# Kernel tuning notes

Hardware: AMD Instinct MI355X
Metric: run time of the kernel (lower is better)

The kernel has to match this reference:

```python
import jax, jax.numpy as jnp
import numpy as np

H = W = 28
NUM_COUNTS = 10  # iteration counts 0..9, one per logit of determine_n


def conv2d(x, w, b=None, pad=2):
    # x: [B,C,H,W], w: [O,I,5,5]
    y = jax.lax.conv_general_dilated(
        x, w, window_strides=(1, 1), padding=[(pad, pad), (pad, pad)],
        dimension_numbers=("NCHW", "OIHW", "NCHW"))
    if b is not None:
        y = y + b[None, :, None, None]
    return y


def maxpool3(x):
    # kernel 3, stride 3, valid: 28 -> 9
    return jax.lax.reduce_window(
        x, -jnp.inf, jax.lax.max,
        window_dimensions=(1, 1, 3, 3), window_strides=(1, 1, 3, 3),
        padding="VALID")


def setup_inputs() -> dict:
    key = jax.random.key(0)
    ks = jax.random.split(key, 8)
    B = 4096
    s = 0.1
    return {
        "x": jax.random.normal(ks[0], (B, H * W), dtype=jnp.float32),
        "w1": jax.random.normal(ks[1], (8, 1, 5, 5), dtype=jnp.float32) * s,
        "b1": jax.random.normal(ks[2], (8,), dtype=jnp.float32) * s,
        "w2": jax.random.normal(ks[3], (16, 8, 5, 5), dtype=jnp.float32) * s,
        "b2": jax.random.normal(ks[4], (16,), dtype=jnp.float32) * s,
        "fcw": jax.random.normal(ks[5], (10, 16 * 9 * 9), dtype=jnp.float32) * s,
        "fcb": jax.random.normal(ks[6], (10,), dtype=jnp.float32) * s,
        "iterw": jax.random.normal(ks[7], (1, 1, 5, 5), dtype=jnp.float32) * s,
    }


def reference(x, w1, b1, w2, b2, fcw, fcb, iterw):
    B = x.shape[0]
    xi = x.reshape(B, 1, H, W)
    # determine_n: CNN router producing 10 logits over iteration counts
    h = jax.nn.relu(conv2d(xi, w1, b1))
    h = jax.nn.relu(conv2d(h, w2, b2))
    h = maxpool3(h).reshape(B, -1)                      # [B, 1296]
    logits = h @ fcw.T + fcb                            # [B, 10]
    probs = jax.nn.softmax(logits, axis=-1)             # [B, 10]
    # smooth TmIter: expected value over f^n(base), n = 0..9
    def step(y, _):
        return conv2d(y, iterw, None), y
    _, ys = jax.lax.scan(step, xi, None, length=NUM_COUNTS)  # [10,B,1,28,28]
    out = jnp.einsum("bn,nbchw->bchw", probs, ys)
    return out.reshape(B, H, W)
```

## Files before the change

kernel.cpp:

```cpp
#include <hip/hip_runtime.h>
#include <hip/hip_bf16.h>
#include <math.h>
#include <float.h>

typedef __fp16 f16x8  __attribute__((ext_vector_type(8)));
typedef __fp16 f16x2  __attribute__((ext_vector_type(2)));
typedef float  f32x16 __attribute__((ext_vector_type(16)));
typedef float  f32x4  __attribute__((ext_vector_type(4)));
typedef unsigned int u32x4 __attribute__((ext_vector_type(4)));
typedef unsigned int u32x2 __attribute__((ext_vector_type(2)));

__device__ inline f16x2 as_h2(unsigned u) { union { unsigned x; f16x2 h; } c; c.x = u; return c.h; }
__device__ inline unsigned pack2(float lo, float hi) {
    union { f16x2 h; unsigned x; } c; c.h[0] = (__fp16)lo; c.h[1] = (__fp16)hi; return c.x;
}
__device__ inline float dot2f(unsigned a, unsigned b, float acc) {
#if __has_builtin(__builtin_amdgcn_fdot2)
    return __builtin_amdgcn_fdot2(as_h2(a), as_h2(b), acc, false);
#else
    f16x2 ah = as_h2(a), bh = as_h2(b);
    return fmaf((float)ah[1], (float)bh[1], fmaf((float)ah[0], (float)bh[0], acc));
#endif
}
#define ALIGN16(hi, lo) __builtin_amdgcn_alignbit((hi), (lo), 16)

#define DY_TAB 0xA524A509A502A540ULL
#define DX_TAB 0x446A444A44924924ULL

__global__ __launch_bounds__(256, 4) void k1_router(
    const float* __restrict__ xg,
    const float* __restrict__ w1g,
    const float* __restrict__ b1g,
    const float* __restrict__ w2g,
    const float* __restrict__ b2g,
    const float* __restrict__ fcwg,
    const float* __restrict__ fcbg,
    float* __restrict__ wsp)
{
    __shared__ __align__(16) char lds[27120];
    char*   spadh  = lds;
    char*   wpk    = lds + 2560;
    __fp16* sh1T   = (__fp16*)(lds + 3200);
    __fp16* sw2t   = (__fp16*)(lds + 20560);
    float*  pooled = (float*)(lds + 20560);
    float*  swred  = (float*)(lds + 26960);

    const int tid  = threadIdx.x;
    const int b    = blockIdx.x;
    const int lane = tid & 63;
    const int wid  = tid >> 6;

    f32x4 z4 = {0.f, 0.f, 0.f, 0.f};
    for (int i = tid; i < 160; i += 256)  ((f32x4*)spadh)[i] = z4;
    for (int i = tid; i < 1085; i += 256) ((f32x4*)sh1T)[i] = z4;
    for (int i = tid; i < 400; i += 256) {
        const int tap = i >> 4, ch = i & 15;
        f16x8 v;
        #pragma unroll
        for (int j = 0; j < 8; ++j) v[j] = (__fp16)w2g[ch * 200 + j * 25 + tap];
        *((f16x8*)(sw2t + i * 8)) = v;
    }
    if (tid < 40) {
        const int r = tid >> 3, c = tid & 7;
        const float* w = w1g + c * 25 + r * 5;
        u32x4 W;
        W.x = pack2(w[0], w[1]); W.y = pack2(w[2], w[3]); W.z = pack2(w[4], 0.f); W.w = 0u;
        *((u32x4*)(wpk + tid * 16)) = W;
    }
    const int yy = tid / 7, q = tid - yy * 7;
    if (tid < 196) {
        f32x4 v = *((const f32x4*)(xg + (size_t)b * 784 + yy * 28 + q * 4));
        unsigned* dst = (unsigned*)(spadh + (yy + 2) * 80 + q * 8 + 4);
        dst[0] = pack2(v[0], v[1]); dst[1] = pack2(v[2], v[3]);
    }
    __syncthreads();

    if (tid < 196) {
        float o[8][4];
        #pragma unroll
        for (int c = 0; c < 8; ++c) {
            const float bv = b1g[c];
            #pragma unroll
            for (int px = 0; px < 4; ++px) o[c][px] = bv;
        }
        #pragma unroll
        for (int r = 0; r < 5; ++r) {
            const char* rowb = spadh + (yy + r) * 80 + q * 8;
            u32x2 A = *((const u32x2*)rowb);
            u32x2 B = *((const u32x2*)(rowb + 8));
            unsigned C0 = *((const unsigned*)(rowb + 16));
            unsigned P[8] = { A.x, ALIGN16(A.y, A.x), A.y, ALIGN16(B.x, A.y),
                              B.x, ALIGN16(B.y, B.x), B.y, ALIGN16(C0,  B.y) };
            #pragma unroll
            for (int c = 0; c < 8; ++c) {
                const u32x4 W = *((const u32x4*)(wpk + (r * 8 + c) * 16));
                #pragma unroll
                for (int px = 0; px < 4; ++px) {
                    float t = o[c][px];
                    t = dot2f(P[px],     W.x, t);
                    t = dot2f(P[px + 2], W.y, t);
                    t = dot2f(P[px + 4], W.z, t);
                    o[c][px] = t;
                }
            }
        }
        #pragma unroll
        for (int px = 0; px < 4; ++px) {
            f16x8 hv;
            #pragma unroll
            for (int c = 0; c < 8; ++c) hv[c] = (__fp16)fmaxf(o[c][px], 0.f);
            *((f16x8*)(sh1T + ((yy + 2) * 35 + (q * 4 + px + 2)) * 8)) = hv;
        }
    }
    const int lr = lane & 31;
    const int g2 = lane >> 5;
    int band = (lr * 57) >> 9; band = band > 2 ? 2 : band;
    const int dy = (int)((DY_TAB >> (2 * lr)) & 3ull);
    const int dx = (int)((DX_TAB >> (2 * lr)) & 3ull);
    const float biasv = (lr < 16) ? b2g[lr] : 0.f;

    f16x8 bfrag[13];
    int   toffB[13];
    #pragma unroll
    for (int s = 0; s < 13; ++s) {
        const int tap = 2 * s + g2;
        const int tapc = tap > 24 ? 24 : tap;
        f16x8 v = *((const f16x8*)(sw2t + (tapc * 16 + (lr & 15)) * 8));
        if (tap > 24 || lr >= 16) {
            #pragma unroll
            for (int j = 0; j < 8; ++j) v[j] = (__fp16)0.f;
        }
        bfrag[s] = v;
        const int ky = (tapc * 13) >> 6;
        const int kx = tapc - 5 * ky;
        toffB[s] = (ky * 35 + kx) * 16;
    }
    __syncthreads();

    auto tileBase = [&](int tile) -> const char* {
        const int cell = tile * 3 + band;
        const int cy = (cell * 57) >> 9, cx = cell - 9 * cy;
        return (const char*)sh1T + ((3 * cy + dy) * 35 + (3 * cx + dx)) * 16;
    };
    auto epi = [&](const f32x16& acc, int tile) {
        float mA, mB, mC;
        if (g2 == 0) {
            mA = fmaxf(fmaxf(fmaxf(acc[0],acc[1]),fmaxf(acc[2],acc[3])), acc[4]);
            mB = fmaxf(fmaxf(fmaxf(acc[5],acc[6]),acc[7]), fmaxf(acc[8],acc[9]));
            mC = fmaxf(fmaxf(fmaxf(acc[10],acc[11]),acc[12]), fmaxf(acc[13],acc[14]));
        } else {
            mA = fmaxf(fmaxf(acc[0],acc[1]),fmaxf(acc[2],acc[3]));
            mB = fmaxf(fmaxf(acc[4],acc[5]),fmaxf(acc[6],acc[7]));
            mC = fmaxf(fmaxf(acc[8],acc[9]),fmaxf(acc[10],acc[11]));
        }
        mA = fmaxf(mA, 0.f); mB = fmaxf(mB, 0.f); mC = fmaxf(mC, 0.f);
        mA = fmaxf(mA, __shfl_xor(mA, 32, 64));
        mB = fmaxf(mB, __shfl_xor(mB, 32, 64));
        mC = fmaxf(mC, __shfl_xor(mC, 32, 64));
        if (g2 == 0 && lr < 16) {
            pooled[lr * 81 + tile * 3 + 0] = mA;
            pooled[lr * 81 + tile * 3 + 1] = mB;
            pooled[lr * 81 + tile * 3 + 2] = mC;
        }
    };
    #pragma unroll 1
    for (int base = wid; base + 4 < 27; base += 8) {
        const char* a0 = tileBase(base);
        const char* a1 = tileBase(base + 4);
        f32x16 acc0, acc1;
        #pragma unroll
        for (int r = 0; r < 16; ++r) { acc0[r] = biasv; acc1[r] = biasv; }
        #pragma unroll
        for (int s = 0; s < 13; ++s) {
            f16x8 af0 = *((const f16x8*)(a0 + toffB[s]));
            f16x8 af1 = *((const f16x8*)(a1 + toffB[s]));
            acc0 = __builtin_amdgcn_mfma_f32_32x32x16_f16(af0, bfrag[s], acc0, 0, 0, 0);
            acc1 = __builtin_amdgcn_mfma_f32_32x32x16_f16(af1, bfrag[s], acc1, 0, 0, 0);
        }
        epi(acc0, base);
        epi(acc1, base + 4);
    }
    if (wid < 3) {
        const int tile = wid + 24;
        const char* a0 = tileBase(tile);
        f32x16 acc;
        #pragma unroll
        for (int r = 0; r < 16; ++r) acc[r] = biasv;
        #pragma unroll
        for (int s = 0; s < 13; ++s) {
            f16x8 af = *((const f16x8*)(a0 + toffB[s]));
            acc = __builtin_amdgcn_mfma_f32_32x32x16_f16(af, bfrag[s], acc, 0, 0, 0);
        }
        epi(acc, tile);
    }
    __syncthreads();

    {
        float part[10];
        #pragma unroll
        for (int j = 0; j < 10; ++j) part[j] = 0.f;
        for (int i4 = tid; i4 < 324; i4 += 256) {
            const f32x4 pv = ((const f32x4*)pooled)[i4];
            #pragma unroll
            for (int j = 0; j < 10; ++j) {
                const f32x4 fw = *((const f32x4*)(fcwg + j * 1296 + i4 * 4));
                part[j] = fmaf(pv[0], fw[0], part[j]);
                part[j] = fmaf(pv[1], fw[1], part[j]);
                part[j] = fmaf(pv[2], fw[2], part[j]);
                part[j] = fmaf(pv[3], fw[3], part[j]);
            }
        }
        #pragma unroll
        for (int j = 0; j < 10; ++j) {
            float v = part[j];
            #pragma unroll
            for (int off = 32; off > 0; off >>= 1) v += __shfl_down(v, off, 64);
            if (lane == 0) swred[wid * 10 + j] = v;
        }
    }
    __syncthreads();

    if (tid == 0) {
        float lg[10]; float mx = -FLT_MAX;
        #pragma unroll
        for (int j = 0; j < 10; ++j) {
            lg[j] = swred[j] + swred[10 + j] + swred[20 + j] + swred[30 + j] + fcbg[j];
            mx = fmaxf(mx, lg[j]);
        }
        float sum = 0.f; float e[10];
        #pragma unroll
        for (int j = 0; j < 10; ++j) { e[j] = expf(lg[j] - mx); sum += e[j]; }
        const float inv = 1.f / sum;
        #pragma unroll
        for (int j = 0; j < 10; ++j) wsp[(size_t)b * 16 + j] = e[j] * inv;
    }
}

__global__ __launch_bounds__(64, 4) void k2_scan(
    const float* __restrict__ xg,
    const float* __restrict__ iwg,
    const float* __restrict__ wsp,
    float* __restrict__ outg)
{
    __shared__ __align__(16) char arena[5120];
    char* bufA = arena;
    char* bufB = arena + 2560;

    const int tid = threadIdx.x;
    const int b   = blockIdx.x;

    f32x4 z4 = {0.f, 0.f, 0.f, 0.f};
    for (int i = tid; i < 320; i += 64) ((f32x4*)arena)[i] = z4;
    __syncthreads();

    for (int i = tid; i < 196; i += 64) {
        const int yy = i / 7, q = i - yy * 7;
        f32x4 v = *((const f32x4*)(xg + (size_t)b * 784 + yy * 28 + q * 4));
        unsigned* dst = (unsigned*)(bufA + (yy + 2) * 80 + q * 8 + 4);
        dst[0] = pack2(v[0], v[1]); dst[1] = pack2(v[2], v[3]);
    }
    __syncthreads();

    unsigned wp[5][3];
    #pragma unroll
    for (int r = 0; r < 5; ++r) {
        wp[r][0] = pack2(iwg[r * 5 + 0], iwg[r * 5 + 1]);
        wp[r][1] = pack2(iwg[r * 5 + 2], iwg[r * 5 + 3]);
        wp[r][2] = pack2(iwg[r * 5 + 4], 0.f);
    }

    const int rq = tid / 7, qq = tid - rq * 7;
    const float p0 = wsp[(size_t)b * 16];
    float accv[16];
    #pragma unroll
    for (int i = 0; i < 16; ++i) accv[i] = 0.f;

    const char* cur = bufA;
    char* nxt = bufB;
    #pragma unroll 1
    for (int n = 1; n <= 9; ++n) {
        const float pn = wsp[(size_t)b * 16 + n];
        if (tid < 49) {
            float v[4][4];
            #pragma unroll
            for (int rr = 0; rr < 4; ++rr)
                #pragma unroll
                for (int px = 0; px < 4; ++px) v[rr][px] = 0.f;
            #pragma unroll
            for (int r = 0; r < 8; ++r) {
                const char* rowb = cur + (4 * rq + r) * 80 + qq * 8;
                u32x2 A = *((const u32x2*)rowb);
                u32x2 B = *((const u32x2*)(rowb + 8));
                unsigned C0 = *((const unsigned*)(rowb + 16));
                unsigned P[8] = { A.x, ALIGN16(A.y, A.x), A.y, ALIGN16(B.x, A.y),
                                  B.x, ALIGN16(B.y, B.x), B.y, ALIGN16(C0,  B.y) };
                if (n == 1 && r >= 2 && r <= 5) {
                    f16x2 t1 = as_h2(A.y), t2 = as_h2(B.x);
                    accv[(r - 2) * 4 + 0] = p0 * (float)t1[0];
                    accv[(r - 2) * 4 + 1] = p0 * (float)t1[1];
                    accv[(r - 2) * 4 + 2] = p0 * (float)t2[0];
                    accv[(r - 2) * 4 + 3] = p0 * (float)t2[1];
                }
                #pragma unroll
                for (int rr = 0; rr < 4; ++rr) {
                    if (rr <= r && r <= rr + 4) {
                        const int ky = r - rr;
                        #pragma unroll
                        for (int px = 0; px < 4; ++px) {
                            float t = v[rr][px];
                            t = dot2f(P[px],     wp[ky][0], t);
                            t = dot2f(P[px + 2], wp[ky][1], t);
                            t = dot2f(P[px + 4], wp[ky][2], t);
                            v[rr][px] = t;
                        }
                    }
                }
            }
            if (n < 9) {
                #pragma unroll
                for (int rr = 0; rr < 4; ++rr) {
                    unsigned* dst = (unsigned*)(nxt + (4 * rq + rr + 2) * 80 + qq * 8 + 4);
                    dst[0] = pack2(v[rr][0], v[rr][1]);
                    dst[1] = pack2(v[rr][2], v[rr][3]);
                }
            }
            #pragma unroll
            for (int rr = 0; rr < 4; ++rr)
                #pragma unroll
                for (int px = 0; px < 4; ++px)
                    accv[rr * 4 + px] = fmaf(pn, v[rr][px], accv[rr * 4 + px]);
        }
        if (n < 9) __syncthreads();
        const char* t = cur; cur = nxt; nxt = (char*)t;
    }

    if (tid < 49) {
        #pragma unroll
        for (int rr = 0; rr < 4; ++rr) {
            f32x4 o = {accv[rr*4], accv[rr*4+1], accv[rr*4+2], accv[rr*4+3]};
            *((f32x4*)(outg + (size_t)b * 784 + (4 * rq + rr) * 28 + qq * 4)) = o;
        }
    }
}

extern "C" void kernel_launch(void* const* d_in, const int* in_sizes, int n_in,
                              void* d_out, int out_size, void* d_ws, size_t ws_size,
                              hipStream_t stream) {
    const float* x   = (const float*)d_in[0];
    const float* w1  = (const float*)d_in[1];
    const float* b1  = (const float*)d_in[2];
    const float* w2  = (const float*)d_in[3];
    const float* b2  = (const float*)d_in[4];
    const float* fcw = (const float*)d_in[5];
    const float* fcb = (const float*)d_in[6];
    const float* iw  = (const float*)d_in[7];
    float* out = (float*)d_out;
    float* wsp = (float*)d_ws;
    const int B = in_sizes[0] / 784;
    k1_router<<<B, 256, 0, stream>>>(x, w1, b1, w2, b2, fcw, fcb, wsp);
    k2_scan<<<B, 64, 0, stream>>>(x, iw, wsp, out);
}
```

Measured before the change: 117.2 us.

## Rework router conv1 to fp32 FMAs, redistribute work per wave, zero only halos

Conv1 in the router kernel switches from packed-fp16 dot2 with LDS-packed weights to plain fp32 FMAs, reading weights from global or scalar memory and the input from an fp32 padded LDS tile. Conv1 work moves from the first 196 threads to 49 lanes in each of the four waves. LDS zeroing now clears only the padding halo rather than the whole buffer, and the conv2 MFMA loop drops the two-tile interleave for a simple one-tile-per-iteration stride. The FC reduction is partitioned so each wave reads its own 81-element slice. The aim is to cut setup and zeroing overhead and balance work across waves, at the cost of more FMA instructions in conv1 and less instruction-level parallelism in the MFMA loop.

```diff
diff --git a/kernel.cpp b/kernel.cpp
--- a/kernel.cpp
+++ b/kernel.cpp
@@ -4,25 +4,9 @@
 #include <float.h>
 
 typedef __fp16 f16x8  __attribute__((ext_vector_type(8)));
-typedef __fp16 f16x2  __attribute__((ext_vector_type(2)));
 typedef float  f32x16 __attribute__((ext_vector_type(16)));
 typedef float  f32x4  __attribute__((ext_vector_type(4)));
-typedef unsigned int u32x4 __attribute__((ext_vector_type(4)));
-typedef unsigned int u32x2 __attribute__((ext_vector_type(2)));
-
-__device__ inline f16x2 as_h2(unsigned u) { union { unsigned x; f16x2 h; } c; c.x = u; return c.h; }
-__device__ inline unsigned pack2(float lo, float hi) {
-    union { f16x2 h; unsigned x; } c; c.h[0] = (__fp16)lo; c.h[1] = (__fp16)hi; return c.x;
-}
-__device__ inline float dot2f(unsigned a, unsigned b, float acc) {
-#if __has_builtin(__builtin_amdgcn_fdot2)
-    return __builtin_amdgcn_fdot2(as_h2(a), as_h2(b), acc, false);
-#else
-    f16x2 ah = as_h2(a), bh = as_h2(b);
-    return fmaf((float)ah[1], (float)bh[1], fmaf((float)ah[0], (float)bh[0], acc));
-#endif
-}
-#define ALIGN16(hi, lo) __builtin_amdgcn_alignbit((hi), (lo), 16)
+typedef float  f32x2  __attribute__((ext_vector_type(2)));
 
 #define DY_TAB 0xA524A509A502A540ULL
 #define DX_TAB 0x446A444A44924924ULL
@@ -37,22 +21,35 @@
     const float* __restrict__ fcbg,
     float* __restrict__ wsp)
 {
-    __shared__ __align__(16) char lds[27120];
-    char*   spadh  = lds;
-    char*   wpk    = lds + 2560;
-    __fp16* sh1T   = (__fp16*)(lds + 3200);
-    __fp16* sw2t   = (__fp16*)(lds + 20560);
-    float*  pooled = (float*)(lds + 20560);
-    float*  swred  = (float*)(lds + 26960);
+    __shared__ __align__(16) char lds[28528];
+    float*  spad   = (float*)(lds + 0);
+    __fp16* sh1T   = (__fp16*)(lds + 4608);
+    __fp16* sw2t   = (__fp16*)(lds + 21968);
+    float*  pooled = (float*)(lds + 21968);
+    float*  swred  = (float*)(lds + 28368);
 
     const int tid  = threadIdx.x;
     const int b    = blockIdx.x;
     const int lane = tid & 63;
     const int wid  = tid >> 6;
 
+    const int ct = wid * 49 + lane;
+    const int yy = ct / 7, q = ct - yy * 7;
+
     f32x4 z4 = {0.f, 0.f, 0.f, 0.f};
-    for (int i = tid; i < 160; i += 256)  ((f32x4*)spadh)[i] = z4;
-    for (int i = tid; i < 1085; i += 256) ((f32x4*)sh1T)[i] = z4;
+    for (int i = tid; i < 92; i += 256) {
+        int row, cu;
+        if (i < 36) { int r = i / 9; cu = i - 9 * r; row = r < 2 ? r : 28 + r; }
+        else        { int j = i - 36; row = 2 + (j >> 1); cu = (j & 1) << 3; }
+        ((f32x4*)spad)[row * 9 + cu] = z4;
+    }
+    for (int i = tid; i < 189; i += 256) {
+        int row, col;
+        if (i < 105) { int r = i / 35; row = (r == 2) ? 30 : r; col = i - 35 * r; }
+        else         { int j = i - 105; row = 2 + j / 3; int cm = j - 3 * (j / 3);
+                       col = (cm == 2) ? 30 : cm; }
+        ((f32x4*)sh1T)[row * 35 + col] = z4;
+    }
     for (int i = tid; i < 400; i += 256) {
         const int tap = i >> 4, ch = i & 15;
         f16x8 v;
@@ -60,22 +57,13 @@
         for (int j = 0; j < 8; ++j) v[j] = (__fp16)w2g[ch * 200 + j * 25 + tap];
         *((f16x8*)(sw2t + i * 8)) = v;
     }
-    if (tid < 40) {
-        const int r = tid >> 3, c = tid & 7;
-        const float* w = w1g + c * 25 + r * 5;
-        u32x4 W;
-        W.x = pack2(w[0], w[1]); W.y = pack2(w[2], w[3]); W.z = pack2(w[4], 0.f); W.w = 0u;
-        *((u32x4*)(wpk + tid * 16)) = W;
-    }
-    const int yy = tid / 7, q = tid - yy * 7;
-    if (tid < 196) {
+    if (lane < 49) {
         f32x4 v = *((const f32x4*)(xg + (size_t)b * 784 + yy * 28 + q * 4));
-        unsigned* dst = (unsigned*)(spadh + (yy + 2) * 80 + q * 8 + 4);
-        dst[0] = pack2(v[0], v[1]); dst[1] = pack2(v[2], v[3]);
-    }
-    __syncthreads();
-
-    if (tid < 196) {
+        *((f32x4*)(spad + (yy + 2) * 36 + q * 4 + 4)) = v;
+    }
+    __syncthreads();
+
+    if (lane < 49) {
         float o[8][4];
         #pragma unroll
         for (int c = 0; c < 8; ++c) {
@@ -85,24 +73,21 @@
         }
         #pragma unroll
         for (int r = 0; r < 5; ++r) {
-            const char* rowb = spadh + (yy + r) * 80 + q * 8;
-            u32x2 A = *((const u32x2*)rowb);
-            u32x2 B = *((const u32x2*)(rowb + 8));
-            unsigned C0 = *((const unsigned*)(rowb + 16));
-            unsigned P[8] = { A.x, ALIGN16(A.y, A.x), A.y, ALIGN16(B.x, A.y),
-                              B.x, ALIGN16(B.y, B.x), B.y, ALIGN16(C0,  B.y) };
-            #pragma unroll
-            for (int c = 0; c < 8; ++c) {
-                const u32x4 W = *((const u32x4*)(wpk + (r * 8 + c) * 16));
-                #pragma unroll
-                for (int px = 0; px < 4; ++px) {
-                    float t = o[c][px];
-                    t = dot2f(P[px],     W.x, t);
-                    t = dot2f(P[px + 2], W.y, t);
-                    t = dot2f(P[px + 4], W.z, t);
-                    o[c][px] = t;
+            const float* rowp = spad + (yy + r) * 36 + q * 4;
+            f32x4 a0 = ((const f32x4*)rowp)[0];
+            f32x4 a1 = ((const f32x4*)rowp)[1];
+            f32x4 a2 = ((const f32x4*)rowp)[2];
+            float u[12] = {a0[0],a0[1],a0[2],a0[3], a1[0],a1[1],a1[2],a1[3],
+                           a2[0],a2[1],a2[2],a2[3]};
+            #pragma unroll
+            for (int c = 0; c < 8; ++c)
+                #pragma unroll
+                for (int kx = 0; kx < 5; ++kx) {
+                    const float w = w1g[c * 25 + r * 5 + kx];
+                    #pragma unroll
+                    for (int px = 0; px < 4; ++px)
+                        o[c][px] = fmaf(u[2 + px + kx], w, o[c][px]);
                 }
-            }
         }
         #pragma unroll
         for (int px = 0; px < 4; ++px) {
@@ -137,12 +122,19 @@
     }
     __syncthreads();
 
-    auto tileBase = [&](int tile) -> const char* {
+    for (int tile = wid; tile < 27; tile += 4) {
         const int cell = tile * 3 + band;
         const int cy = (cell * 57) >> 9, cx = cell - 9 * cy;
-        return (const char*)sh1T + ((3 * cy + dy) * 35 + (3 * cx + dx)) * 16;
-    };
-    auto epi = [&](const f32x16& acc, int tile) {
+        const int R0 = 3 * cy + dy, C0 = 3 * cx + dx;
+        const char* abase = (const char*)sh1T + (R0 * 35 + C0) * 16;
+        f32x16 acc;
+        #pragma unroll
+        for (int r = 0; r < 16; ++r) acc[r] = biasv;
+        #pragma unroll
+        for (int s = 0; s < 13; ++s) {
+            f16x8 af = *((const f16x8*)(abase + toffB[s]));
+            acc = __builtin_amdgcn_mfma_f32_32x32x16_f16(af, bfrag[s], acc, 0, 0, 0);
+        }
         float mA, mB, mC;
         if (g2 == 0) {
             mA = fmaxf(fmaxf(fmaxf(acc[0],acc[1]),fmaxf(acc[2],acc[3])), acc[4]);
@@ -162,36 +154,6 @@
             pooled[lr * 81 + tile * 3 + 1] = mB;
             pooled[lr * 81 + tile * 3 + 2] = mC;
         }
-    };
-    #pragma unroll 1
-    for (int base = wid; base + 4 < 27; base += 8) {
-        const char* a0 = tileBase(base);
-        const char* a1 = tileBase(base + 4);
-        f32x16 acc0, acc1;
-        #pragma unroll
-        for (int r = 0; r < 16; ++r) { acc0[r] = biasv; acc1[r] = biasv; }
-        #pragma unroll
-        for (int s = 0; s < 13; ++s) {
-            f16x8 af0 = *((const f16x8*)(a0 + toffB[s]));
-            f16x8 af1 = *((const f16x8*)(a1 + toffB[s]));
-            acc0 = __builtin_amdgcn_mfma_f32_32x32x16_f16(af0, bfrag[s], acc0, 0, 0, 0);
-            acc1 = __builtin_amdgcn_mfma_f32_32x32x16_f16(af1, bfrag[s], acc1, 0, 0, 0);
-        }
-        epi(acc0, base);
-        epi(acc1, base + 4);
-    }
-    if (wid < 3) {
-        const int tile = wid + 24;
-        const char* a0 = tileBase(tile);
-        f32x16 acc;
-        #pragma unroll
-        for (int r = 0; r < 16; ++r) acc[r] = biasv;
-        #pragma unroll
-        for (int s = 0; s < 13; ++s) {
-            f16x8 af = *((const f16x8*)(a0 + toffB[s]));
-            acc = __builtin_amdgcn_mfma_f32_32x32x16_f16(af, bfrag[s], acc, 0, 0, 0);
-        }
-        epi(acc, tile);
     }
     __syncthreads();
 
@@ -199,7 +161,8 @@
         float part[10];
         #pragma unroll
         for (int j = 0; j < 10; ++j) part[j] = 0.f;
-        for (int i4 = tid; i4 < 324; i4 += 256) {
+        const int i4e = wid * 81 + 81;
+        for (int i4 = wid * 81 + lane; i4 < i4e; i4 += 64) {
             const f32x4 pv = ((const f32x4*)pooled)[i4];
             #pragma unroll
             for (int j = 0; j < 10; ++j) {
@@ -235,6 +198,23 @@
         for (int j = 0; j < 10; ++j) wsp[(size_t)b * 16 + j] = e[j] * inv;
     }
 }
+
+typedef __fp16 f16x2  __attribute__((ext_vector_type(2)));
+typedef unsigned int u32x2 __attribute__((ext_vector_type(2)));
+
+__device__ inline f16x2 as_h2(unsigned u) { union { unsigned x; f16x2 h; } c; c.x = u; return c.h; }
+__device__ inline unsigned pack2(float lo, float hi) {
+    union { f16x2 h; unsigned x; } c; c.h[0] = (__fp16)lo; c.h[1] = (__fp16)hi; return c.x;
+}
+__device__ inline float dot2f(unsigned a, unsigned b, float acc) {
+#if __has_builtin(__builtin_amdgcn_fdot2)
+    return __builtin_amdgcn_fdot2(as_h2(a), as_h2(b), acc, false);
+#else
+    f16x2 ah = as_h2(a), bh = as_h2(b);
+    return fmaf((float)ah[1], (float)bh[1], fmaf((float)ah[0], (float)bh[0], acc));
+#endif
+}
+#define ALIGN16(hi, lo) __builtin_amdgcn_alignbit((hi), (lo), 16)
 
 __global__ __launch_bounds__(64, 4) void k2_scan(
     const float* __restrict__ xg,
```

New measurement: 113.8 us. -2.9%, faster.
